# Kernel optimization log

Hardware: AMD Instinct MI355X
Metric: run time of the kernel (lower is better)

## Reference

```python
import jax, jax.numpy as jnp
import numpy as np

DIM = 2048
H = 16
KV_RANK = 512
NOPE = 128
ROPE_D = 64
VD = 128
QK = NOPE + ROPE_D  # 192
SCALE = QK ** -0.5
B, S = 2, 2048
EPS = 1e-5


def _rope(x, start_pos):
    # x: (b, s, h, d) or (b, s, d); rotate along last dim, positions along axis 1
    s = x.shape[1]
    d = x.shape[-1]
    half = d // 2
    inv_freq = 1.0 / (10000.0 ** (jnp.arange(half, dtype=jnp.float32) * (2.0 / d)))
    pos = jnp.arange(start_pos, start_pos + s, dtype=jnp.float32)
    ang = pos[:, None] * inv_freq[None, :]  # (s, half)
    cos, sin = jnp.cos(ang), jnp.sin(ang)
    if x.ndim == 4:
        cos, sin = cos[None, :, None, :], sin[None, :, None, :]
    else:
        cos, sin = cos[None, :, :], sin[None, :, :]
    x1, x2 = x[..., :half], x[..., half:]
    return jnp.concatenate([x1 * cos - x2 * sin, x2 * cos + x1 * sin], axis=-1).astype(x.dtype)


def _layernorm(x, w, b):
    mu = jnp.mean(x, axis=-1, keepdims=True)
    var = jnp.mean(jnp.square(x - mu), axis=-1, keepdims=True)
    return (x - mu) * jax.lax.rsqrt(var + EPS) * w + b


def setup_inputs() -> dict:
    key = jax.random.key(0)
    ks = jax.random.split(key, 6)
    std = 0.02
    x = jax.random.normal(ks[0], (B, S, DIM), dtype=jnp.float32)
    wq = jax.random.normal(ks[1], (H * QK, DIM), dtype=jnp.float32) * std
    wkv_a = jax.random.normal(ks[2], (KV_RANK + ROPE_D, DIM), dtype=jnp.float32) * std
    wkv_b = jax.random.normal(ks[3], (H * (NOPE + VD), KV_RANK), dtype=jnp.float32) * std
    wo = jax.random.normal(ks[4], (DIM, H * VD), dtype=jnp.float32) * std
    kv_norm_w = jnp.ones((KV_RANK,), dtype=jnp.float32)
    kv_norm_b = jnp.zeros((KV_RANK,), dtype=jnp.float32)
    return {"x": x, "wq": wq, "wkv_a": wkv_a, "kv_norm_w": kv_norm_w,
            "kv_norm_b": kv_norm_b, "wkv_b": wkv_b, "wo": wo, "start_pos": 0}


def reference(x, wq, wkv_a, kv_norm_w, kv_norm_b, wkv_b, wo, start_pos):
    b, s, _ = x.shape
    # query projection: (b,s,H,QK)
    q = (x @ wq.T).reshape(b, s, H, QK)
    q_nope, q_pe = q[..., :NOPE], q[..., NOPE:]
    q_pe = _rope(q_pe, start_pos)
    # compressed kv + rope key
    kv_all = x @ wkv_a.T                      # (b,s,KV_RANK+ROPE_D)
    kv, k_pe = kv_all[..., :KV_RANK], kv_all[..., KV_RANK:]
    k_pe = _rope(k_pe, start_pos)             # (b,s,ROPE_D)
    kvn = _layernorm(kv, kv_norm_w, kv_norm_b)  # (b,s,KV_RANK)
    # absorb path: expand compressed kv through per-head wkv_b blocks
    w = wkv_b.reshape(H, NOPE + VD, KV_RANK)
    k_nope = jnp.einsum('btc,hdc->bthd', kvn, w[:, :NOPE])   # (b,t,H,NOPE)
    v = jnp.einsum('btc,hdc->bthd', kvn, w[:, NOPE:])        # (b,t,H,VD)
    q_full = jnp.concatenate([q_nope, q_pe], axis=-1)        # (b,s,H,QK)
    k_full = jnp.concatenate(
        [k_nope, jnp.broadcast_to(k_pe[:, :, None, :], (b, s, H, ROPE_D))], axis=-1)
    scores = jnp.einsum('bshd,bthd->bhst', q_full, k_full) * SCALE
    causal = jnp.tril(jnp.ones((s, s), dtype=bool))
    scores = jnp.where(causal[None, None], scores, jnp.float32(-1e30))
    attn = jax.nn.softmax(scores, axis=-1)
    out = jnp.einsum('bhst,bthd->bshd', attn, v).reshape(b, s, H * VD)
    return out @ wo.T
```

## Files before the change

### kernel.cpp

```cpp
#include <hip/hip_runtime.h>
#include <hip/hip_bf16.h>
#include <math.h>

typedef __bf16 bf16_t;
typedef __bf16 bf16x4 __attribute__((ext_vector_type(4)));
typedef __bf16 bf16x8 __attribute__((ext_vector_type(8)));
typedef float f32x4 __attribute__((ext_vector_type(4)));

#define SEQ 2048
#define MLA_SCALE 0.07216878364870322f
#define LN_EPS 1e-5f

__device__ __forceinline__ void gload_lds16(const bf16_t* g, bf16_t* l) {
    __builtin_amdgcn_global_load_lds(
        (const __attribute__((address_space(1))) uint32_t*)(const void*)g,
        (__attribute__((address_space(3))) uint32_t*)(void*)l, 16, 0, 0);
}

__global__ __launch_bounds__(256)
void cvt_f32_bf16(const float* __restrict__ in, bf16_t* __restrict__ out, int n4) {
    for (int i = blockIdx.x * 256 + threadIdx.x; i < n4; i += gridDim.x * 256) {
        float4 v = ((const float4*)in)[i];
        bf16x4 p = { (bf16_t)v.x, (bf16_t)v.y, (bf16_t)v.z, (bf16_t)v.w };
        ((bf16x4*)out)[i] = p;
    }
}

#define G256_PHASE(TAU, KS, MH, HTO, MAT, WAITV)                               \
{                                                                              \
    const int slot_ = (2 * (TAU) + (KS)) & 3;                                  \
    bf16x8 af_[4];                                                             \
    {                                                                          \
        const bf16_t* ab_ = As + slot_ * 8192 +                                \
                            (wm2 * 128 + (MH) * 64 + lr) * 32 + rdcol;         \
        _Pragma("unroll")                                                      \
        for (int f = 0; f < 4; ++f) af_[f] = *(const bf16x8*)(ab_ + f * 512);  \
    }                                                                          \
    if ((MH) == 0) {                                                           \
        const bf16_t* bb_ = Bs + slot_ * 8192 + (wn2 * 64 + lr) * 32 + rdcol;  \
        _Pragma("unroll")                                                      \
        for (int f = 0; f < 4; ++f) bq[f] = *(const bf16x8*)(bb_ + f * 512);   \
    }                                                                          \
    if ((MAT) == 0) stageA(2 * T + 3 + (HTO)); else stageB(2 * T + 3 + (HTO)); \
    __builtin_amdgcn_s_barrier();                                              \
    asm volatile("" ::: "memory");                                             \
    __builtin_amdgcn_s_setprio(1);                                             \
    _Pragma("unroll")                                                          \
    for (int f = 0; f < 4; ++f)                                                \
        _Pragma("unroll")                                                      \
        for (int n = 0; n < 4; ++n)                                            \
            acc[(MH) * 4 + f][n] = __builtin_amdgcn_mfma_f32_16x16x32_bf16(    \
                af_[f], bq[n], acc[(MH) * 4 + f][n], 0, 0, 0);                 \
    __builtin_amdgcn_s_setprio(0);                                             \
    asm volatile("" ::: "memory");                                             \
    if (WAITV) asm volatile("s_waitcnt vmcnt(8)" ::: "memory");                \
    __builtin_amdgcn_s_barrier();                                              \
}

template<bool PACK>
__global__ __launch_bounds__(512, 2)
void gemm256(const bf16_t* __restrict__ A, const bf16_t* __restrict__ B,
             float* __restrict__ C, bf16_t* __restrict__ kpack,
             bf16_t* __restrict__ vt, int N, int K) {
    __shared__ __attribute__((aligned(16))) bf16_t As[32768];
    __shared__ __attribute__((aligned(16))) bf16_t Bs[32768];
    __shared__ __attribute__((aligned(16))) bf16_t Ds[8192];

    const int tid = threadIdx.x;
    const int lane = tid & 63, w = tid >> 6;
    const int lr = lane & 15, kh = lane >> 4;
    const int wm2 = w >> 2, wn2 = w & 3;
    const int bm = blockIdx.y, bn = blockIdx.x;
    const int NT = K >> 6;

    const int rdcol = 8 * (kh ^ ((lr >> 1) & 3));
    const int strow = (w << 5) + (lane >> 2);
    const int scol = 8 * ((lane & 3) ^ ((lane >> 3) & 3));

    f32x4 acc[8][4];
    #pragma unroll
    for (int i = 0; i < 8; ++i)
        #pragma unroll
        for (int j = 0; j < 4; ++j) acc[i][j] = 0.0f;

    auto stageA = [&](int ht) {
        int hs = (ht < 2 * NT) ? ht : (2 * NT - 1);
        int tau = hs >> 1, kap = hs & 1;
        const bf16_t* g = A + (size_t)(bm * 256 + strow) * K + tau * 64 + kap * 32 + scol;
        bf16_t* l = (ht < 2 * NT) ? (As + (ht & 3) * 8192 + w * 1024) : (Ds + w * 1024);
        gload_lds16(g, l);
        gload_lds16(g + (size_t)16 * K, l + 512);
    };
    auto stageB = [&](int ht) {
        int hs = (ht < 2 * NT) ? ht : (2 * NT - 1);
        int tau = hs >> 1, kap = hs & 1;
        const bf16_t* g = B + (size_t)(bn * 256 + strow) * K + tau * 64 + kap * 32 + scol;
        bf16_t* l = (ht < 2 * NT) ? (Bs + (ht & 3) * 8192 + w * 1024) : (Ds + w * 1024);
        gload_lds16(g, l);
        gload_lds16(g + (size_t)16 * K, l + 512);
    };

    stageA(0); stageB(0); stageA(1); stageB(1); stageA(2); stageB(2);
    asm volatile("s_waitcnt vmcnt(8)" ::: "memory");
    __builtin_amdgcn_s_barrier();

    for (int it = 0; it < (NT >> 1); ++it) {
        const int T = 2 * it;
        bf16x8 bq[4];
        G256_PHASE(T,     0, 0, 0, 0, 0)
        G256_PHASE(T,     0, 1, 0, 1, 1)
        G256_PHASE(T,     1, 0, 1, 0, 0)
        G256_PHASE(T,     1, 1, 1, 1, 1)
        G256_PHASE(T + 1, 0, 0, 2, 0, 0)
        G256_PHASE(T + 1, 0, 1, 2, 1, 1)
        G256_PHASE(T + 1, 1, 0, 3, 0, 0)
        G256_PHASE(T + 1, 1, 1, 3, 1, 1)
    }

    const int rg = kh * 4;
    if (!PACK) {
        #pragma unroll
        for (int mf = 0; mf < 8; ++mf)
            #pragma unroll
            for (int nf = 0; nf < 4; ++nf) {
                size_t row0 = (size_t)(bm * 256 + wm2 * 128 + mf * 16 + rg);
                int col = bn * 256 + wn2 * 64 + nf * 16 + lr;
                #pragma unroll
                for (int rr = 0; rr < 4; ++rr)
                    C[(row0 + rr) * N + col] = acc[mf][nf][rr];
            }
    } else {
        const int h = bn;
        #pragma unroll
        for (int mf = 0; mf < 8; ++mf)
            #pragma unroll
            for (int nf = 0; nf < 4; ++nf) {
                int d = wn2 * 64 + nf * 16 + lr;
                int trow = bm * 256 + wm2 * 128 + mf * 16 + rg;
                int b = trow >> 11, t = trow & 2047;
                if (d < 128) {
                    bf16_t* p = kpack + ((size_t)(b * 16 + h) * SEQ + t) * 192 + d;
                    #pragma unroll
                    for (int rr = 0; rr < 4; ++rr)
                        p[rr * 192] = (bf16_t)acc[mf][nf][rr];
                } else {
                    bf16x4 pv = { (bf16_t)acc[mf][nf][0], (bf16_t)acc[mf][nf][1],
                                  (bf16_t)acc[mf][nf][2], (bf16_t)acc[mf][nf][3] };
                    *(bf16x4*)(vt + ((size_t)(b * 16 + h) * 128 + (d - 128)) * SEQ + t) = pv;
                }
            }
    }
}

__device__ __forceinline__ void gemm_core(const bf16_t* __restrict__ A,
                                          const bf16_t* __restrict__ B,
                                          int N, int K, int bm, int bn,
                                          bf16_t* As, bf16_t* Bs,
                                          f32x4 (&acc)[4][4]) {
    const int tid = threadIdx.x;
    const int lane = tid & 63, w = tid >> 6;
    const int lr = lane & 15, kh = lane >> 4;
    const int wm = (w >> 1) * 64, wn = (w & 1) * 64;
    const int subrow = lane >> 2;
    const int colel = (lane & 3) * 8;

    const int rA = bm * 128 + 32 * w + subrow;
    const int rB = bn * 128 + 32 * w + subrow;
    const int rb1 = (rB < N) ? rB : (N - 1);
    const int rb2 = (rB + 16 < N) ? (rB + 16) : (N - 1);

    for (int kt = 0; kt < K; kt += 32) {
        __syncthreads();
        gload_lds16(A + (size_t)rA * K + kt + colel,        As + (2 * w) * 512);
        gload_lds16(A + (size_t)(rA + 16) * K + kt + colel, As + (2 * w + 1) * 512);
        gload_lds16(B + (size_t)rb1 * K + kt + colel,       Bs + (2 * w) * 512);
        gload_lds16(B + (size_t)rb2 * K + kt + colel,       Bs + (2 * w + 1) * 512);
        __syncthreads();
        bf16x8 af[4], bfr[4];
        #pragma unroll
        for (int im = 0; im < 4; ++im)
            af[im] = *(const bf16x8*)(As + (wm + im * 16 + lr) * 32 + kh * 8);
        #pragma unroll
        for (int jn = 0; jn < 4; ++jn)
            bfr[jn] = *(const bf16x8*)(Bs + (wn + jn * 16 + lr) * 32 + kh * 8);
        #pragma unroll
        for (int im = 0; im < 4; ++im)
            #pragma unroll
            for (int jn = 0; jn < 4; ++jn)
                acc[im][jn] = __builtin_amdgcn_mfma_f32_16x16x32_bf16(
                    af[im], bfr[jn], acc[im][jn], 0, 0, 0);
    }
}

__global__ __launch_bounds__(256)
void gemm_nt(const bf16_t* __restrict__ A, const bf16_t* __restrict__ B,
             float* __restrict__ C, int M, int N, int K) {
    __shared__ bf16_t As[4096], Bs[4096];
    f32x4 acc[4][4];
    #pragma unroll
    for (int i = 0; i < 4; ++i)
        #pragma unroll
        for (int j = 0; j < 4; ++j) acc[i][j] = 0.0f;
    gemm_core(A, B, N, K, blockIdx.y, blockIdx.x, As, Bs, acc);

    const int tid = threadIdx.x, lane = tid & 63, w = tid >> 6;
    const int lr = lane & 15, rg = (lane >> 4) * 4;
    const int wm = (w >> 1) * 64, wn = (w & 1) * 64;
    #pragma unroll
    for (int im = 0; im < 4; ++im)
        #pragma unroll
        for (int jn = 0; jn < 4; ++jn) {
            int col = blockIdx.x * 128 + wn + jn * 16 + lr;
            if (col >= N) continue;
            size_t rowb = (size_t)(blockIdx.y * 128 + wm + im * 16 + rg);
            #pragma unroll
            for (int rr = 0; rr < 4; ++rr)
                C[(rowb + rr) * N + col] = acc[im][jn][rr];
        }
}

__global__ __launch_bounds__(256)
void rope_ln(float* __restrict__ q, const float* __restrict__ kv_all,
             const float* __restrict__ lnw, const float* __restrict__ lnb,
             bf16_t* __restrict__ kvnb, bf16_t* __restrict__ kpack,
             const int* __restrict__ start_pos) {
    const int m = blockIdx.x;
    const int tid = threadIdx.x;
    const int b = m >> 11, t = m & 2047;
    const float pos = (float)(start_pos[0] + t);
    __shared__ float red[8];
    __shared__ float stats[2];
    __shared__ float kbuf[64];

    const float* kvrow = kv_all + (size_t)m * 576;
    float v0 = kvrow[tid], v1 = kvrow[tid + 256];
    float ssum = v0 + v1, ssq = v0 * v0 + v1 * v1;
    for (int off = 32; off > 0; off >>= 1) {
        ssum += __shfl_down(ssum, off);
        ssq  += __shfl_down(ssq, off);
    }
    const int lane = tid & 63, wid = tid >> 6;
    if (lane == 0) { red[wid] = ssum; red[4 + wid] = ssq; }
    __syncthreads();
    if (tid == 0) {
        float ts = red[0] + red[1] + red[2] + red[3];
        float tq = red[4] + red[5] + red[6] + red[7];
        float mu = ts * (1.0f / 512.0f);
        float var = tq * (1.0f / 512.0f) - mu * mu;
        stats[0] = mu;
        stats[1] = rsqrtf(var + LN_EPS);
    }
    if (tid < 32) {
        int j = tid;
        float inv = expf(-(float)j * 0.2878231366242554f);
        float ang = pos * inv;
        float c = cosf(ang), sn = sinf(ang);
        float x1 = kvrow[512 + j], x2 = kvrow[544 + j];
        kbuf[j]      = x1 * c - x2 * sn;
        kbuf[32 + j] = x2 * c + x1 * sn;
    }
    __syncthreads();
    float mu = stats[0], rstd = stats[1];
    kvnb[(size_t)m * 512 + tid]       = (bf16_t)((v0 - mu) * rstd * lnw[tid] + lnb[tid]);
    kvnb[(size_t)m * 512 + tid + 256] = (bf16_t)((v1 - mu) * rstd * lnw[tid + 256] + lnb[tid + 256]);

    {
        int hh = tid >> 4, j4 = (tid & 15) * 4;
        bf16x4 pk = { (bf16_t)kbuf[j4], (bf16_t)kbuf[j4 + 1],
                      (bf16_t)kbuf[j4 + 2], (bf16_t)kbuf[j4 + 3] };
        *(bf16x4*)(kpack + ((size_t)(b * 16 + hh) * SEQ + t) * 192 + 128 + j4) = pk;
    }
    #pragma unroll
    for (int i = 0; i < 2; ++i) {
        int p = tid + 256 * i;
        int h = p >> 5, j = p & 31;
        float inv = expf(-(float)j * 0.2878231366242554f);
        float ang = pos * inv;
        float c = cosf(ang), sn = sinf(ang);
        size_t base = (size_t)m * 3072 + h * 192 + 128;
        float x1 = q[base + j], x2 = q[base + 32 + j];
        q[base + j]      = x1 * c - x2 * sn;
        q[base + 32 + j] = x2 * c + x1 * sn;
    }
}

__global__ __launch_bounds__(256, 2)
void attn_mfma(const float* __restrict__ q, const bf16_t* __restrict__ kpack,
               const bf16_t* __restrict__ vt, bf16_t* __restrict__ ao) {
    __shared__ bf16_t Ks[64][200];
    __shared__ bf16_t Vts[128][72];
    __shared__ bf16_t Pls[4][16][72];

    const int bx = blockIdx.x, h = blockIdx.y, b = blockIdx.z;
    const int tid = threadIdx.x;
    const int lane = tid & 63, w = tid >> 6;
    const int lr = lane & 15, kh = lane >> 4;
    const size_t bS = (size_t)b * SEQ;
    const bf16_t* kbase = kpack + (size_t)(b * 16 + h) * SEQ * 192;
    const bf16_t* vbase = vt + (size_t)(b * 16 + h) * 128 * SEQ;

    int krow_[6], koff_[6], vd_[4], vt8_[4];
    #pragma unroll
    for (int i = 0; i < 6; ++i) { int c = tid + 256 * i; krow_[i] = c / 24; koff_[i] = (c % 24) * 8; }
    #pragma unroll
    for (int i = 0; i < 4; ++i) { int c = tid + 256 * i; vd_[i] = c >> 3; vt8_[i] = (c & 7) * 8; }

    for (int half = 0; half < 2; ++half) {
        const int qt = half ? bx : (31 - bx);
        const int q0 = qt * 64;
        const int myrow = q0 + w * 16;

        bf16x8 qf[6];
        {
            const float* qrow = q + (bS + myrow + lr) * 3072 + h * 192;
            #pragma unroll
            for (int ks = 0; ks < 6; ++ks) {
                float4 a = *(const float4*)(qrow + ks * 32 + kh * 8);
                float4 c2 = *(const float4*)(qrow + ks * 32 + kh * 8 + 4);
                qf[ks][0] = (bf16_t)a.x;  qf[ks][1] = (bf16_t)a.y;
                qf[ks][2] = (bf16_t)a.z;  qf[ks][3] = (bf16_t)a.w;
                qf[ks][4] = (bf16_t)c2.x; qf[ks][5] = (bf16_t)c2.y;
                qf[ks][6] = (bf16_t)c2.z; qf[ks][7] = (bf16_t)c2.w;
            }
        }

        f32x4 O[8];
        #pragma unroll
        for (int i = 0; i < 8; ++i) O[i] = 0.0f;
        float m_r[4] = { -1e30f, -1e30f, -1e30f, -1e30f };
        float l_r[4] = { 0.0f, 0.0f, 0.0f, 0.0f };

        bf16x8 rk[6], rv[4];
        #pragma unroll
        for (int i = 0; i < 6; ++i)
            rk[i] = *(const bf16x8*)(kbase + (size_t)krow_[i] * 192 + koff_[i]);
        #pragma unroll
        for (int i = 0; i < 4; ++i)
            rv[i] = *(const bf16x8*)(vbase + (size_t)vd_[i] * SEQ + vt8_[i]);

        for (int kt = 0; kt <= qt; ++kt) {
            __syncthreads();
            #pragma unroll
            for (int i = 0; i < 6; ++i) *(bf16x8*)&Ks[krow_[i]][koff_[i]] = rk[i];
            #pragma unroll
            for (int i = 0; i < 4; ++i) *(bf16x8*)&Vts[vd_[i]][vt8_[i]] = rv[i];
            if (kt < qt) {
                const int t1 = (kt + 1) * 64;
                #pragma unroll
                for (int i = 0; i < 6; ++i)
                    rk[i] = *(const bf16x8*)(kbase + (size_t)(t1 + krow_[i]) * 192 + koff_[i]);
                #pragma unroll
                for (int i = 0; i < 4; ++i)
                    rv[i] = *(const bf16x8*)(vbase + (size_t)vd_[i] * SEQ + t1 + vt8_[i]);
            }
            __syncthreads();

            f32x4 sacc[4];
            #pragma unroll
            for (int j = 0; j < 4; ++j) sacc[j] = 0.0f;
            __builtin_amdgcn_s_setprio(1);
            #pragma unroll
            for (int ks = 0; ks < 6; ++ks)
                #pragma unroll
                for (int j = 0; j < 4; ++j) {
                    bf16x8 bfr = *(const bf16x8*)&Ks[j * 16 + lr][ks * 32 + kh * 8];
                    sacc[j] = __builtin_amdgcn_mfma_f32_16x16x32_bf16(qf[ks], bfr, sacc[j], 0, 0, 0);
                }
            __builtin_amdgcn_s_setprio(0);

            const int t0 = kt * 64;
            float sv[4][4];
            if (kt == qt) {
                #pragma unroll
                for (int j = 0; j < 4; ++j) {
                    int tcol = t0 + j * 16 + lr;
                    #pragma unroll
                    for (int rr = 0; rr < 4; ++rr) {
                        int qrow2 = myrow + kh * 4 + rr;
                        sv[j][rr] = (tcol > qrow2) ? -1e30f : sacc[j][rr] * MLA_SCALE;
                    }
                }
            } else {
                #pragma unroll
                for (int j = 0; j < 4; ++j)
                    #pragma unroll
                    for (int rr = 0; rr < 4; ++rr)
                        sv[j][rr] = sacc[j][rr] * MLA_SCALE;
            }

            float corr[4];
            #pragma unroll
            for (int rr = 0; rr < 4; ++rr) {
                float mx = fmaxf(fmaxf(sv[0][rr], sv[1][rr]), fmaxf(sv[2][rr], sv[3][rr]));
                mx = fmaxf(mx, __shfl_xor(mx, 1));
                mx = fmaxf(mx, __shfl_xor(mx, 2));
                mx = fmaxf(mx, __shfl_xor(mx, 4));
                mx = fmaxf(mx, __shfl_xor(mx, 8));
                float mnew = fmaxf(m_r[rr], mx);
                float cr = __expf(m_r[rr] - mnew);
                float ps = 0.0f;
                #pragma unroll
                for (int j = 0; j < 4; ++j) {
                    float p = __expf(sv[j][rr] - mnew);
                    sv[j][rr] = p;
                    ps += p;
                }
                ps += __shfl_xor(ps, 1);
                ps += __shfl_xor(ps, 2);
                ps += __shfl_xor(ps, 4);
                ps += __shfl_xor(ps, 8);
                l_r[rr] = l_r[rr] * cr + ps;
                m_r[rr] = mnew;
                corr[rr] = cr;
            }
            #pragma unroll
            for (int dt = 0; dt < 8; ++dt)
                #pragma unroll
                for (int rr = 0; rr < 4; ++rr)
                    O[dt][rr] *= corr[rr];

            #pragma unroll
            for (int rr = 0; rr < 4; ++rr)
                #pragma unroll
                for (int j = 0; j < 4; ++j)
                    Pls[w][kh * 4 + rr][j * 16 + lr] = (bf16_t)sv[j][rr];
            bf16x8 pa0 = *(const bf16x8*)&Pls[w][lr][kh * 8];
            bf16x8 pa1 = *(const bf16x8*)&Pls[w][lr][32 + kh * 8];
            __builtin_amdgcn_s_setprio(1);
            #pragma unroll
            for (int dt = 0; dt < 8; ++dt) {
                bf16x8 b0 = *(const bf16x8*)&Vts[dt * 16 + lr][kh * 8];
                O[dt] = __builtin_amdgcn_mfma_f32_16x16x32_bf16(pa0, b0, O[dt], 0, 0, 0);
                bf16x8 b1 = *(const bf16x8*)&Vts[dt * 16 + lr][32 + kh * 8];
                O[dt] = __builtin_amdgcn_mfma_f32_16x16x32_bf16(pa1, b1, O[dt], 0, 0, 0);
            }
            __builtin_amdgcn_s_setprio(0);
        }

        #pragma unroll
        for (int rr = 0; rr < 4; ++rr) {
            float inv = 1.0f / l_r[rr];
            size_t rowb = (bS + myrow + kh * 4 + rr) * 2048 + h * 128;
            #pragma unroll
            for (int dt = 0; dt < 8; ++dt)
                ao[rowb + dt * 16 + lr] = (bf16_t)(O[dt][rr] * inv);
        }
    }
}

extern "C" void kernel_launch(void* const* d_in, const int* in_sizes, int n_in,
                              void* d_out, int out_size, void* d_ws, size_t ws_size,
                              hipStream_t stream) {
    const float* x     = (const float*)d_in[0];
    const float* wq    = (const float*)d_in[1];
    const float* wkv_a = (const float*)d_in[2];
    const float* lnw   = (const float*)d_in[3];
    const float* lnb   = (const float*)d_in[4];
    const float* wkv_b = (const float*)d_in[5];
    const float* wo    = (const float*)d_in[6];
    const int* start_pos = (const int*)d_in[7];
    float* out = (float*)d_out;

    char* w8 = (char*)d_ws;
    bf16_t* xb   = (bf16_t*)(w8);
    bf16_t* wqb  = (bf16_t*)(w8 + 16777216);
    bf16_t* wab  = (bf16_t*)(w8 + 29360128);
    bf16_t* wbb  = (bf16_t*)(w8 + 31719424);
    bf16_t* wob  = (bf16_t*)(w8 + 35913728);
    bf16_t* kvnb = (bf16_t*)(w8 + 44302336);
    bf16_t* kpk  = (bf16_t*)(w8 + 48496640);
    bf16_t* vtb  = (bf16_t*)(w8 + 73662464);
    bf16_t* aob  = (bf16_t*)(w8 + 90439680);
    float*  qws  = (float*)(w8 + 107216896);
    float*  kva  = (float*)(w8 + 157548544);

    cvt_f32_bf16<<<2048, 256, 0, stream>>>(x,     xb,  8388608 / 4);
    cvt_f32_bf16<<<2048, 256, 0, stream>>>(wq,    wqb, 6291456 / 4);
    cvt_f32_bf16<<<1152, 256, 0, stream>>>(wkv_a, wab, 1179648 / 4);
    cvt_f32_bf16<<<2048, 256, 0, stream>>>(wkv_b, wbb, 2097152 / 4);
    cvt_f32_bf16<<<2048, 256, 0, stream>>>(wo,    wob, 4194304 / 4);

    gemm256<false><<<dim3(12, 16), 512, 0, stream>>>(xb, wqb, qws, nullptr, nullptr, 3072, 2048);
    gemm_nt<<<dim3(5, 32), 256, 0, stream>>>(xb, wab, kva, 4096, 576, 2048);
    rope_ln<<<4096, 256, 0, stream>>>(qws, kva, lnw, lnb, kvnb, kpk, start_pos);
    gemm256<true><<<dim3(16, 16), 512, 0, stream>>>(kvnb, wbb, nullptr, kpk, vtb, 4096, 512);
    attn_mfma<<<dim3(16, 16, 2), 256, 0, stream>>>(qws, kpk, vtb, aob);
    gemm_nt<<<dim3(16, 32), 256, 0, stream>>>(aob, wob, out, 4096, 2048, 2048);
}
```

Before: 331.5 us.

## Emit bf16 head-major Q from GEMM, fuse q rope into attention, transpose score MFMA

The Q projection GEMM now writes bf16 output directly in a per-head (b,h,t,192) layout instead of fp32 row-major. The query RoPE moves out of rope_ln: rope_ln stores a cos/sin table, and attention applies the rotation when it loads q fragments. The score MFMA swaps its operands so each lane holds a whole query row, which makes the softmax max/sum reductions in-lane plus two cross-lane shuffles instead of four shuffles per row. Together these cut fp32 Q traffic and the read-modify-write pass over Q. The cost is strided bf16 stores in the GEMM epilogue and a few extra shuffles to broadcast the correction factors.

```diff
diff --git a/kernel.cpp b/kernel.cpp
--- a/kernel.cpp
+++ b/kernel.cpp
@@ -3,6 +3,7 @@
 #include <math.h>
 
 typedef __bf16 bf16_t;
+typedef __bf16 bf16x2 __attribute__((ext_vector_type(2)));
 typedef __bf16 bf16x4 __attribute__((ext_vector_type(4)));
 typedef __bf16 bf16x8 __attribute__((ext_vector_type(8)));
 typedef float f32x4 __attribute__((ext_vector_type(4)));
@@ -57,11 +58,11 @@
     __builtin_amdgcn_s_barrier();                                              \
 }
 
-template<bool PACK>
+template<int MODE>
 __global__ __launch_bounds__(512, 2)
 void gemm256(const bf16_t* __restrict__ A, const bf16_t* __restrict__ B,
-             float* __restrict__ C, bf16_t* __restrict__ kpack,
-             bf16_t* __restrict__ vt, int N, int K) {
+             float* __restrict__ C, bf16_t* __restrict__ out0,
+             bf16_t* __restrict__ out1, int N, int K) {
     __shared__ __attribute__((aligned(16))) bf16_t As[32768];
     __shared__ __attribute__((aligned(16))) bf16_t Bs[32768];
     __shared__ __attribute__((aligned(16))) bf16_t Ds[8192];
@@ -118,7 +119,7 @@
     }
 
     const int rg = kh * 4;
-    if (!PACK) {
+    if (MODE == 0) {
         #pragma unroll
         for (int mf = 0; mf < 8; ++mf)
             #pragma unroll
@@ -129,7 +130,7 @@
                 for (int rr = 0; rr < 4; ++rr)
                     C[(row0 + rr) * N + col] = acc[mf][nf][rr];
             }
-    } else {
+    } else if (MODE == 1) {
         const int h = bn;
         #pragma unroll
         for (int mf = 0; mf < 8; ++mf)
@@ -139,15 +140,29 @@
                 int trow = bm * 256 + wm2 * 128 + mf * 16 + rg;
                 int b = trow >> 11, t = trow & 2047;
                 if (d < 128) {
-                    bf16_t* p = kpack + ((size_t)(b * 16 + h) * SEQ + t) * 192 + d;
+                    bf16_t* p = out0 + ((size_t)(b * 16 + h) * SEQ + t) * 192 + d;
                     #pragma unroll
                     for (int rr = 0; rr < 4; ++rr)
                         p[rr * 192] = (bf16_t)acc[mf][nf][rr];
                 } else {
                     bf16x4 pv = { (bf16_t)acc[mf][nf][0], (bf16_t)acc[mf][nf][1],
                                   (bf16_t)acc[mf][nf][2], (bf16_t)acc[mf][nf][3] };
-                    *(bf16x4*)(vt + ((size_t)(b * 16 + h) * 128 + (d - 128)) * SEQ + t) = pv;
+                    *(bf16x4*)(out1 + ((size_t)(b * 16 + h) * 128 + (d - 128)) * SEQ + t) = pv;
                 }
+            }
+    } else {
+        #pragma unroll
+        for (int mf = 0; mf < 8; ++mf)
+            #pragma unroll
+            for (int nf = 0; nf < 4; ++nf) {
+                int n = bn * 256 + wn2 * 64 + nf * 16 + lr;
+                int h = n / 192, d = n - h * 192;
+                int trow = bm * 256 + wm2 * 128 + mf * 16 + rg;
+                int b = trow >> 11, t = trow & 2047;
+                bf16_t* p = out0 + ((size_t)(b * 16 + h) * SEQ + t) * 192 + d;
+                #pragma unroll
+                for (int rr = 0; rr < 4; ++rr)
+                    p[rr * 192] = (bf16_t)acc[mf][nf][rr];
             }
     }
 }
@@ -220,10 +235,10 @@
 }
 
 __global__ __launch_bounds__(256)
-void rope_ln(float* __restrict__ q, const float* __restrict__ kv_all,
+void rope_ln(const float* __restrict__ kv_all,
              const float* __restrict__ lnw, const float* __restrict__ lnb,
              bf16_t* __restrict__ kvnb, bf16_t* __restrict__ kpack,
-             const int* __restrict__ start_pos) {
+             float2* __restrict__ rope_cs, const int* __restrict__ start_pos) {
     const int m = blockIdx.x;
     const int tid = threadIdx.x;
     const int b = m >> 11, t = m & 2047;
@@ -258,6 +273,7 @@
         float x1 = kvrow[512 + j], x2 = kvrow[544 + j];
         kbuf[j]      = x1 * c - x2 * sn;
         kbuf[32 + j] = x2 * c + x1 * sn;
+        if (b == 0) rope_cs[t * 32 + j] = make_float2(c, sn);
     }
     __syncthreads();
     float mu = stats[0], rstd = stats[1];
@@ -270,23 +286,12 @@
                       (bf16_t)kbuf[j4 + 2], (bf16_t)kbuf[j4 + 3] };
         *(bf16x4*)(kpack + ((size_t)(b * 16 + hh) * SEQ + t) * 192 + 128 + j4) = pk;
     }
-    #pragma unroll
-    for (int i = 0; i < 2; ++i) {
-        int p = tid + 256 * i;
-        int h = p >> 5, j = p & 31;
-        float inv = expf(-(float)j * 0.2878231366242554f);
-        float ang = pos * inv;
-        float c = cosf(ang), sn = sinf(ang);
-        size_t base = (size_t)m * 3072 + h * 192 + 128;
-        float x1 = q[base + j], x2 = q[base + 32 + j];
-        q[base + j]      = x1 * c - x2 * sn;
-        q[base + 32 + j] = x2 * c + x1 * sn;
-    }
 }
 
 __global__ __launch_bounds__(256, 2)
-void attn_mfma(const float* __restrict__ q, const bf16_t* __restrict__ kpack,
-               const bf16_t* __restrict__ vt, bf16_t* __restrict__ ao) {
+void attn_mfma(const bf16_t* __restrict__ qb, const bf16_t* __restrict__ kpack,
+               const bf16_t* __restrict__ vt, const float2* __restrict__ rope_cs,
+               bf16_t* __restrict__ ao) {
     __shared__ bf16_t Ks[64][200];
     __shared__ bf16_t Vts[128][72];
     __shared__ bf16_t Pls[4][16][72];
@@ -309,26 +314,28 @@
         const int qt = half ? bx : (31 - bx);
         const int q0 = qt * 64;
         const int myrow = q0 + w * 16;
+        const int qabs = myrow + lr;
 
         bf16x8 qf[6];
         {
-            const float* qrow = q + (bS + myrow + lr) * 3072 + h * 192;
-            #pragma unroll
-            for (int ks = 0; ks < 6; ++ks) {
-                float4 a = *(const float4*)(qrow + ks * 32 + kh * 8);
-                float4 c2 = *(const float4*)(qrow + ks * 32 + kh * 8 + 4);
-                qf[ks][0] = (bf16_t)a.x;  qf[ks][1] = (bf16_t)a.y;
-                qf[ks][2] = (bf16_t)a.z;  qf[ks][3] = (bf16_t)a.w;
-                qf[ks][4] = (bf16_t)c2.x; qf[ks][5] = (bf16_t)c2.y;
-                qf[ks][6] = (bf16_t)c2.z; qf[ks][7] = (bf16_t)c2.w;
+            const bf16_t* qrow = qb + ((size_t)(b * 16 + h) * SEQ + qabs) * 192;
+            #pragma unroll
+            for (int ks = 0; ks < 6; ++ks)
+                qf[ks] = *(const bf16x8*)(qrow + ks * 32 + kh * 8);
+            const float2* csp = rope_cs + (size_t)qabs * 32 + kh * 8;
+            #pragma unroll
+            for (int i = 0; i < 8; ++i) {
+                float2 cs = csp[i];
+                float x1 = (float)qf[4][i], x2 = (float)qf[5][i];
+                qf[4][i] = (bf16_t)(x1 * cs.x - x2 * cs.y);
+                qf[5][i] = (bf16_t)(x2 * cs.x + x1 * cs.y);
             }
         }
 
         f32x4 O[8];
         #pragma unroll
         for (int i = 0; i < 8; ++i) O[i] = 0.0f;
-        float m_r[4] = { -1e30f, -1e30f, -1e30f, -1e30f };
-        float l_r[4] = { 0.0f, 0.0f, 0.0f, 0.0f };
+        float m_r = -1e30f, l_r = 0.0f;
 
         bf16x8 rk[6], rv[4];
         #pragma unroll
@@ -363,56 +370,51 @@
             for (int ks = 0; ks < 6; ++ks)
                 #pragma unroll
                 for (int j = 0; j < 4; ++j) {
-                    bf16x8 bfr = *(const bf16x8*)&Ks[j * 16 + lr][ks * 32 + kh * 8];
-                    sacc[j] = __builtin_amdgcn_mfma_f32_16x16x32_bf16(qf[ks], bfr, sacc[j], 0, 0, 0);
+                    bf16x8 kf = *(const bf16x8*)&Ks[j * 16 + lr][ks * 32 + kh * 8];
+                    sacc[j] = __builtin_amdgcn_mfma_f32_16x16x32_bf16(kf, qf[ks], sacc[j], 0, 0, 0);
                 }
             __builtin_amdgcn_s_setprio(0);
 
             const int t0 = kt * 64;
-            float sv[4][4];
+            float p[16];
             if (kt == qt) {
                 #pragma unroll
-                for (int j = 0; j < 4; ++j) {
-                    int tcol = t0 + j * 16 + lr;
+                for (int j = 0; j < 4; ++j)
                     #pragma unroll
                     for (int rr = 0; rr < 4; ++rr) {
-                        int qrow2 = myrow + kh * 4 + rr;
-                        sv[j][rr] = (tcol > qrow2) ? -1e30f : sacc[j][rr] * MLA_SCALE;
+                        int tabs = t0 + j * 16 + kh * 4 + rr;
+                        p[j * 4 + rr] = (tabs > qabs) ? -1e30f : sacc[j][rr] * MLA_SCALE;
                     }
-                }
             } else {
                 #pragma unroll
                 for (int j = 0; j < 4; ++j)
                     #pragma unroll
                     for (int rr = 0; rr < 4; ++rr)
-                        sv[j][rr] = sacc[j][rr] * MLA_SCALE;
-            }
+                        p[j * 4 + rr] = sacc[j][rr] * MLA_SCALE;
+            }
+
+            float mx = p[0];
+            #pragma unroll
+            for (int e = 1; e < 16; ++e) mx = fmaxf(mx, p[e]);
+            mx = fmaxf(mx, __shfl_xor(mx, 16));
+            mx = fmaxf(mx, __shfl_xor(mx, 32));
+            float mnew = fmaxf(m_r, mx);
+            float cr = __expf(m_r - mnew);
+            float ps = 0.0f;
+            #pragma unroll
+            for (int e = 0; e < 16; ++e) {
+                p[e] = __expf(p[e] - mnew);
+                ps += p[e];
+            }
+            ps += __shfl_xor(ps, 16);
+            ps += __shfl_xor(ps, 32);
+            l_r = l_r * cr + ps;
+            m_r = mnew;
 
             float corr[4];
             #pragma unroll
-            for (int rr = 0; rr < 4; ++rr) {
-                float mx = fmaxf(fmaxf(sv[0][rr], sv[1][rr]), fmaxf(sv[2][rr], sv[3][rr]));
-                mx = fmaxf(mx, __shfl_xor(mx, 1));
-                mx = fmaxf(mx, __shfl_xor(mx, 2));
-                mx = fmaxf(mx, __shfl_xor(mx, 4));
-                mx = fmaxf(mx, __shfl_xor(mx, 8));
-                float mnew = fmaxf(m_r[rr], mx);
-                float cr = __expf(m_r[rr] - mnew);
-                float ps = 0.0f;
-                #pragma unroll
-                for (int j = 0; j < 4; ++j) {
-                    float p = __expf(sv[j][rr] - mnew);
-                    sv[j][rr] = p;
-                    ps += p;
-                }
-                ps += __shfl_xor(ps, 1);
-                ps += __shfl_xor(ps, 2);
-                ps += __shfl_xor(ps, 4);
-                ps += __shfl_xor(ps, 8);
-                l_r[rr] = l_r[rr] * cr + ps;
-                m_r[rr] = mnew;
-                corr[rr] = cr;
-            }
+            for (int rr = 0; rr < 4; ++rr)
+                corr[rr] = __shfl(cr, kh * 4 + rr);
             #pragma unroll
             for (int dt = 0; dt < 8; ++dt)
                 #pragma unroll
@@ -420,10 +422,12 @@
                     O[dt][rr] *= corr[rr];
 
             #pragma unroll
-            for (int rr = 0; rr < 4; ++rr)
-                #pragma unroll
-                for (int j = 0; j < 4; ++j)
-                    Pls[w][kh * 4 + rr][j * 16 + lr] = (bf16_t)sv[j][rr];
+            for (int j = 0; j < 4; ++j)
+                #pragma unroll
+                for (int rr2 = 0; rr2 < 2; ++rr2) {
+                    bf16x2 pp = { (bf16_t)p[j * 4 + 2 * rr2], (bf16_t)p[j * 4 + 2 * rr2 + 1] };
+                    *(bf16x2*)&Pls[w][lr][j * 16 + kh * 4 + 2 * rr2] = pp;
+                }
             bf16x8 pa0 = *(const bf16x8*)&Pls[w][lr][kh * 8];
             bf16x8 pa1 = *(const bf16x8*)&Pls[w][lr][32 + kh * 8];
             __builtin_amdgcn_s_setprio(1);
@@ -437,13 +441,16 @@
             __builtin_amdgcn_s_setprio(0);
         }
 
+        float linv[4];
+        #pragma unroll
+        for (int rr = 0; rr < 4; ++rr)
+            linv[rr] = 1.0f / __shfl(l_r, kh * 4 + rr);
         #pragma unroll
         for (int rr = 0; rr < 4; ++rr) {
-            float inv = 1.0f / l_r[rr];
             size_t rowb = (bS + myrow + kh * 4 + rr) * 2048 + h * 128;
             #pragma unroll
             for (int dt = 0; dt < 8; ++dt)
-                ao[rowb + dt * 16 + lr] = (bf16_t)(O[dt][rr] * inv);
+                ao[rowb + dt * 16 + lr] = (bf16_t)(O[dt][rr] * linv[rr]);
         }
     }
 }
@@ -471,8 +478,9 @@
     bf16_t* kpk  = (bf16_t*)(w8 + 48496640);
     bf16_t* vtb  = (bf16_t*)(w8 + 73662464);
     bf16_t* aob  = (bf16_t*)(w8 + 90439680);
-    float*  qws  = (float*)(w8 + 107216896);
-    float*  kva  = (float*)(w8 + 157548544);
+    bf16_t* qbh  = (bf16_t*)(w8 + 107216896);
+    float*  kva  = (float*)(w8 + 132382720);
+    float2* rcs  = (float2*)(w8 + 141819904);
 
     cvt_f32_bf16<<<2048, 256, 0, stream>>>(x,     xb,  8388608 / 4);
     cvt_f32_bf16<<<2048, 256, 0, stream>>>(wq,    wqb, 6291456 / 4);
@@ -480,10 +488,10 @@
     cvt_f32_bf16<<<2048, 256, 0, stream>>>(wkv_b, wbb, 2097152 / 4);
     cvt_f32_bf16<<<2048, 256, 0, stream>>>(wo,    wob, 4194304 / 4);
 
-    gemm256<false><<<dim3(12, 16), 512, 0, stream>>>(xb, wqb, qws, nullptr, nullptr, 3072, 2048);
+    gemm256<2><<<dim3(12, 16), 512, 0, stream>>>(xb, wqb, nullptr, qbh, nullptr, 3072, 2048);
     gemm_nt<<<dim3(5, 32), 256, 0, stream>>>(xb, wab, kva, 4096, 576, 2048);
-    rope_ln<<<4096, 256, 0, stream>>>(qws, kva, lnw, lnb, kvnb, kpk, start_pos);
-    gemm256<true><<<dim3(16, 16), 512, 0, stream>>>(kvnb, wbb, nullptr, kpk, vtb, 4096, 512);
-    attn_mfma<<<dim3(16, 16, 2), 256, 0, stream>>>(qws, kpk, vtb, aob);
+    rope_ln<<<4096, 256, 0, stream>>>(kva, lnw, lnb, kvnb, kpk, rcs, start_pos);
+    gemm256<1><<<dim3(16, 16), 512, 0, stream>>>(kvnb, wbb, nullptr, kpk, vtb, 4096, 512);
+    attn_mfma<<<dim3(16, 16, 2), 256, 0, stream>>>(qbh, kpk, vtb, rcs, aob);
     gemm_nt<<<dim3(16, 32), 256, 0, stream>>>(aob, wob, out, 4096, 2048, 2048);
 }
```

After: 308.5 us. 6.9% less time.
